# Kernel tuning notes

Measured on AMD Instinct MI355X. Metric: run time of the kernel, lower is better.

The kernel has to match this reference:

```python
import jax, jax.numpy as jnp
import numpy as np

WS = 12      # window_size
OV = 6       # overlap
STEP = WS - OV
EPS = 1e-5   # LayerNorm eps (torch default)


def setup_inputs() -> dict:
    key = jax.random.key(0)
    ks = jax.random.split(key, 6)
    B, L, H, Dh = 4, 4092, 8, 64
    d_model = H * Dh
    sc = 1.0 / np.sqrt(Dh)
    return {
        "queries": jax.random.normal(ks[0], (B, L, H, Dh), dtype=jnp.float32),
        "keys": jax.random.normal(ks[1], (B, L, H, Dh), dtype=jnp.float32),
        "values": jax.random.normal(ks[2], (B, L, H, Dh), dtype=jnp.float32),
        "Wq": jax.random.normal(ks[3], (Dh, Dh), dtype=jnp.float32) * sc,
        "Wk": jax.random.normal(ks[4], (Dh, Dh), dtype=jnp.float32) * sc,
        "Wv": jax.random.normal(ks[5], (Dh, Dh), dtype=jnp.float32) * sc,
        "gamma": jnp.ones((d_model,), dtype=jnp.float32),
        "beta": jnp.zeros((d_model,), dtype=jnp.float32),
    }


def reference(queries, keys, values, Wq, Wk, Wv, gamma, beta):
    # input layout: [B, L, H, Dh]
    B, L, H, Dh = queries.shape
    nw = (L - OV) // STEP                       # number of windows
    Lc = WS + STEP * (nw - 1)                   # reconstructed length (== L)
    idx = jnp.arange(nw)[:, None] * STEP + jnp.arange(WS)[None, :]  # [nw, WS]

    def windows(x):
        # [B,L,H,Dh] -> [B,H,nw,WS,Dh]
        return jnp.transpose(x, (0, 2, 1, 3))[:, :, idx, :]

    qw, kw, vw = windows(queries), windows(keys), windows(values)
    # per-head-dim linear projections (nn.Linear: x @ W.T)
    Q = jnp.einsum('bhnwd,ed->bhnwe', qw, Wq)
    K = jnp.einsum('bhnwd,ed->bhnwe', kw, Wk)
    V = jnp.einsum('bhnwd,ed->bhnwe', vw, Wv)

    scores = jnp.einsum('bhnqd,bhnkd->bhnqk', Q, K) / jnp.sqrt(jnp.asarray(Dh, Q.dtype))
    attn = jax.nn.softmax(scores, axis=-1)      # [B,H,nw,WS,WS]
    ow = jnp.einsum('bhnqk,bhnkd->bhnqd', attn, V)

    # [B,H,nw,WS,Dh] -> [B,nw,WS,H*Dh]
    attn_out = jnp.transpose(ow, (0, 2, 3, 1, 4)).reshape(B, nw, WS, H * Dh)

    # overlap-add + averaging
    flat_idx = idx.reshape(-1)                  # [nw*WS]
    acc = jnp.zeros((B, Lc, H * Dh), dtype=attn_out.dtype)
    acc = acc.at[:, flat_idx, :].add(attn_out.reshape(B, nw * WS, H * Dh))
    cnt = jnp.zeros((Lc,), dtype=attn_out.dtype).at[flat_idx].add(1.0)
    out = acc / cnt[None, :, None]

    # residual + LayerNorm
    resid = queries.reshape(B, L, H * Dh)
    x = out + resid
    mu = jnp.mean(x, axis=-1, keepdims=True)
    var = jnp.mean((x - mu) ** 2, axis=-1, keepdims=True)
    z = (x - mu) / jnp.sqrt(var + EPS) * gamma + beta
    return z, attn
```

## Files before the change

kernel.cpp:

```cpp
#include <hip/hip_runtime.h>
#include <math.h>

#define B_    4
#define L_    4092
#define H_    8
#define DM    512
#define WS_   12
#define NW    681
#define NC    682
#define EPS_  1e-5f
#define Z_ELEMS (B_*L_*DM)
#define NQUAD 32736

typedef unsigned short u16;

__device__ __forceinline__ u16 f2bf(float f) {
    union { float f; unsigned u; } x; x.f = f;
    unsigned u = x.u;
    return (u16)((u + 0x7FFFu + ((u >> 16) & 1u)) >> 16);
}
__device__ __forceinline__ float bf2f(u16 h) {
    union { unsigned u; float f; } x; x.u = ((unsigned)h) << 16; return x.f;
}

__global__ __launch_bounds__(256) void proj_kernel(
    const float* __restrict__ q, const float* __restrict__ k, const float* __restrict__ v,
    const float* __restrict__ Wq, const float* __restrict__ Wk, const float* __restrict__ Wv,
    float* __restrict__ Qf, float* __restrict__ Kf, u16* __restrict__ Vh)
{
    const int tensor = blockIdx.y;
    const float* __restrict__ X = (tensor == 0) ? q  : (tensor == 1) ? k  : v;
    const float* __restrict__ W = (tensor == 0) ? Wq : (tensor == 1) ? Wk : Wv;
    float* __restrict__ Yf      = (tensor == 0) ? Qf : Kf;
    const bool isV = (tensor == 2);

    const int t = threadIdx.x, lane = t & 63, wv = t >> 6;

    float4 wr[16];
    #pragma unroll
    for (int j = 0; j < 16; ++j)
        wr[j] = *(const float4*)(W + lane * 64 + j * 4);

    __shared__ alignas(16) float Xw[4][4][64];

    const int li = lane >> 4;
    const int lc = (lane & 15) * 4;

    const int waveId = blockIdx.x * 4 + wv;
    for (int qd = waveId; qd < NQUAD; qd += 2048) {
        const int rbase = qd * 4;
        const int r = rbase + li;
        const int bh = r / L_;
        const int l = r - bh * L_;
        const int b = bh >> 3, h = bh & 7;
        const float4 xf = *(const float4*)(X + (((size_t)b * L_ + l) * H_ + h) * 64 + lc);
        *(float4*)&Xw[wv][li][lc] = xf;

        float acc0 = 0.f, acc1 = 0.f, acc2 = 0.f, acc3 = 0.f;
        #pragma unroll
        for (int d4 = 0; d4 < 16; ++d4) {
            const float4 w4 = wr[d4];
            const float4 x0 = *(const float4*)&Xw[wv][0][d4 * 4];
            const float4 x1 = *(const float4*)&Xw[wv][1][d4 * 4];
            const float4 x2 = *(const float4*)&Xw[wv][2][d4 * 4];
            const float4 x3 = *(const float4*)&Xw[wv][3][d4 * 4];
            acc0 += x0.x*w4.x + x0.y*w4.y + x0.z*w4.z + x0.w*w4.w;
            acc1 += x1.x*w4.x + x1.y*w4.y + x1.z*w4.z + x1.w*w4.w;
            acc2 += x2.x*w4.x + x2.y*w4.y + x2.z*w4.z + x2.w*w4.w;
            acc3 += x3.x*w4.x + x3.y*w4.y + x3.z*w4.z + x3.w*w4.w;
        }

        const size_t orow = (size_t)rbase * 64 + lane;
        if (!isV) {
            Yf[orow]       = acc0;
            Yf[orow + 64]  = acc1;
            Yf[orow + 128] = acc2;
            Yf[orow + 192] = acc3;
        } else {
            Vh[orow]       = f2bf(acc0);
            Vh[orow + 64]  = f2bf(acc1);
            Vh[orow + 128] = f2bf(acc2);
            Vh[orow + 192] = f2bf(acc3);
        }
    }
}

__global__ __launch_bounds__(512, 4) void attn_ln_kernel(
    const float* __restrict__ Qf, const float* __restrict__ Kf, const u16* __restrict__ Vh,
    const float* __restrict__ qres, const float* __restrict__ gamma,
    const float* __restrict__ beta, float* __restrict__ attn, float* __restrict__ z)
{
    __shared__ alignas(16) float Ks[8][18][64];
    __shared__ alignas(16) float Vsf[8][18][64];

    const int c = blockIdx.x, b = blockIdx.y;
    const int t = threadIdx.x, lane = t & 63, h = t >> 6;
    const int qq = lane >> 2, ks = lane & 3;
    const int bh = b * 8 + h;
    const int lbase = c * 6 - 6;

    for (int i = t; i < 2304; i += 512) {
        const int hh  = i / 288;
        const int rem = i - hh * 288;
        const int rr  = rem >> 4;
        const int cc  = (rem & 15) * 4;
        const int l = lbase + rr;
        float4 kf4 = make_float4(0.f, 0.f, 0.f, 0.f);
        float4 vf4 = make_float4(0.f, 0.f, 0.f, 0.f);
        if (l >= 0 && l < L_) {
            const size_t base = ((size_t)(b * 8 + hh) * L_ + l) * 64 + cc;
            kf4 = *(const float4*)(Kf + base);
            const ushort4 u4 = *(const ushort4*)(Vh + base);
            vf4.x = bf2f(u4.x); vf4.y = bf2f(u4.y); vf4.z = bf2f(u4.z); vf4.w = bf2f(u4.w);
        }
        *(float4*)&Ks[hh][rr][cc]  = kf4;
        *(float4*)&Vsf[hh][rr][cc] = vf4;
    }
    __syncthreads();

    const bool hasA = (c < NW), hasB = (c > 0);
    const float scale = (hasA && hasB) ? 0.5f : 1.0f;

    float4 qs0, qs1, qs2, qs3;
    const int qmax = hasA ? 12 : 6;
    if (qq < qmax) {
        const float* qp = Qf + ((size_t)bh * L_ + (c * 6 + qq)) * 64 + ks * 16;
        qs0 = *(const float4*)(qp);     qs1 = *(const float4*)(qp + 4);
        qs2 = *(const float4*)(qp + 8); qs3 = *(const float4*)(qp + 12);
    } else {
        qs0 = qs1 = qs2 = qs3 = make_float4(0.f, 0.f, 0.f, 0.f);
    }

    float s[18];
    #pragma unroll
    for (int kt = 0; kt < 18; ++kt) {
        const float* kp = &Ks[h][kt][ks * 16];
        const float4 k0 = *(const float4*)(kp);
        const float4 k1 = *(const float4*)(kp + 4);
        const float4 k2 = *(const float4*)(kp + 8);
        const float4 k3 = *(const float4*)(kp + 12);
        s[kt] = qs0.x*k0.x + qs0.y*k0.y + qs0.z*k0.z + qs0.w*k0.w
              + qs1.x*k1.x + qs1.y*k1.y + qs1.z*k1.z + qs1.w*k1.w
              + qs2.x*k2.x + qs2.y*k2.y + qs2.z*k2.z + qs2.w*k2.w
              + qs3.x*k3.x + qs3.y*k3.y + qs3.z*k3.z + qs3.w*k3.w;
    }
    #pragma unroll
    for (int kt = 0; kt < 18; ++kt) {
        s[kt] += __shfl_xor(s[kt], 1);
        s[kt] += __shfl_xor(s[kt], 2);
    }

    float eA[12], invA = 0.f;
    if (hasA) {
        float mxA = s[6];
        #pragma unroll
        for (int j = 1; j < 12; ++j) mxA = fmaxf(mxA, s[6 + j]);
        float sumA = 0.f;
        #pragma unroll
        for (int j = 0; j < 12; ++j) { eA[j] = __expf((s[6 + j] - mxA) * 0.125f); sumA += eA[j]; }
        invA = 1.0f / sumA;
        if (ks == 0 && qq < 12) {
            float* ao = attn + ((size_t)bh * NW + c) * 144 + qq * 12;
            float4 a0, a1, a2;
            a0.x = eA[0]*invA; a0.y = eA[1]*invA;  a0.z = eA[2]*invA;  a0.w = eA[3]*invA;
            a1.x = eA[4]*invA; a1.y = eA[5]*invA;  a1.z = eA[6]*invA;  a1.w = eA[7]*invA;
            a2.x = eA[8]*invA; a2.y = eA[9]*invA;  a2.z = eA[10]*invA; a2.w = eA[11]*invA;
            *(float4*)(ao)     = a0;
            *(float4*)(ao + 4) = a1;
            *(float4*)(ao + 8) = a2;
        }
    } else {
        #pragma unroll
        for (int j = 0; j < 12; ++j) eA[j] = 0.f;
    }

    float eB[12], invB = 0.f;
    if (hasB) {
        float mxB = s[0];
        #pragma unroll
        for (int j = 1; j < 12; ++j) mxB = fmaxf(mxB, s[j]);
        float sumB = 0.f;
        #pragma unroll
        for (int j = 0; j < 12; ++j) { eB[j] = __expf((s[j] - mxB) * 0.125f); sumB += eB[j]; }
        invB = 1.0f / sumB;
    } else {
        #pragma unroll
        for (int j = 0; j < 12; ++j) eB[j] = 0.f;
    }

    float4 xo0 = make_float4(0.f,0.f,0.f,0.f), xo1 = xo0, xo2 = xo0, xo3 = xo0;
    if (qq < 6) {
        #pragma unroll
        for (int kt = 0; kt < 18; ++kt) {
            const float wa = (kt >= 6) ? eA[kt - 6] * invA : 0.f;
            const float wb = (kt < 12) ? eB[kt] * invB : 0.f;
            const float wk = scale * (wa + wb);
            const float* vp = &Vsf[h][kt][ks * 16];
            const float4 v0 = *(const float4*)(vp);
            const float4 v1 = *(const float4*)(vp + 4);
            const float4 v2 = *(const float4*)(vp + 8);
            const float4 v3 = *(const float4*)(vp + 12);
            xo0.x += wk*v0.x; xo0.y += wk*v0.y; xo0.z += wk*v0.z; xo0.w += wk*v0.w;
            xo1.x += wk*v1.x; xo1.y += wk*v1.y; xo1.z += wk*v1.z; xo1.w += wk*v1.w;
            xo2.x += wk*v2.x; xo2.y += wk*v2.y; xo2.z += wk*v2.z; xo2.w += wk*v2.w;
            xo3.x += wk*v3.x; xo3.y += wk*v3.y; xo3.z += wk*v3.z; xo3.w += wk*v3.w;
        }
    }
    __syncthreads();

    float* Xs = &Ks[0][0][0];
    if (qq < 6) {
        float* xp = Xs + qq * 516 + h * 64 + ks * 16;
        *(float4*)(xp)      = xo0;
        *(float4*)(xp + 4)  = xo1;
        *(float4*)(xp + 8)  = xo2;
        *(float4*)(xp + 12) = xo3;
    }
    __syncthreads();

    if (h < 6) {
        const int l = c * 6 + h;
        const int cc = lane * 8;
        float4 xa = *(const float4*)(Xs + h * 516 + cc);
        float4 xb = *(const float4*)(Xs + h * 516 + cc + 4);
        const float* qr = qres + ((size_t)b * L_ + l) * DM + cc;
        const float4 ra  = *(const float4*)qr;
        const float4 rb2 = *(const float4*)(qr + 4);
        xa.x += ra.x;  xa.y += ra.y;  xa.z += ra.z;  xa.w += ra.w;
        xb.x += rb2.x; xb.y += rb2.y; xb.z += rb2.z; xb.w += rb2.w;

        float s1 = xa.x + xa.y + xa.z + xa.w + xb.x + xb.y + xb.z + xb.w;
        float s2 = xa.x*xa.x + xa.y*xa.y + xa.z*xa.z + xa.w*xa.w
                 + xb.x*xb.x + xb.y*xb.y + xb.z*xb.z + xb.w*xb.w;
        #pragma unroll
        for (int off = 1; off < 64; off <<= 1) {
            s1 += __shfl_xor(s1, off, 64);
            s2 += __shfl_xor(s2, off, 64);
        }
        const float mu  = s1 * (1.0f / 512.0f);
        const float var = s2 * (1.0f / 512.0f) - mu * mu;
        const float inv = 1.0f / sqrtf(var + EPS_);

        const float4 ga = *(const float4*)(gamma + cc);
        const float4 gb = *(const float4*)(gamma + cc + 4);
        const float4 ba = *(const float4*)(beta + cc);
        const float4 bb = *(const float4*)(beta + cc + 4);
        float4 oa, ob;
        oa.x = (xa.x - mu) * inv * ga.x + ba.x;
        oa.y = (xa.y - mu) * inv * ga.y + ba.y;
        oa.z = (xa.z - mu) * inv * ga.z + ba.z;
        oa.w = (xa.w - mu) * inv * ga.w + ba.w;
        ob.x = (xb.x - mu) * inv * gb.x + bb.x;
        ob.y = (xb.y - mu) * inv * gb.y + bb.y;
        ob.z = (xb.z - mu) * inv * gb.z + bb.z;
        ob.w = (xb.w - mu) * inv * gb.w + bb.w;
        float* zp = z + ((size_t)b * L_ + l) * DM + cc;
        *(float4*)zp = oa;
        *(float4*)(zp + 4) = ob;
    }
}

extern "C" void kernel_launch(void* const* d_in, const int* in_sizes, int n_in,
                              void* d_out, int out_size, void* d_ws, size_t ws_size,
                              hipStream_t stream) {
    const float* q     = (const float*)d_in[0];
    const float* k     = (const float*)d_in[1];
    const float* v     = (const float*)d_in[2];
    const float* Wq    = (const float*)d_in[3];
    const float* Wk    = (const float*)d_in[4];
    const float* Wv    = (const float*)d_in[5];
    const float* gamma = (const float*)d_in[6];
    const float* beta  = (const float*)d_in[7];

    float* z    = (float*)d_out;
    float* attn = (float*)d_out + Z_ELEMS;

    const size_t plane = (size_t)B_ * H_ * L_ * 64;
    float* Qf = (float*)d_ws;
    float* Kf = Qf + plane;
    u16*  Vh  = (u16*)(Kf + plane);

    proj_kernel<<<dim3(512, 3, 1), 256, 0, stream>>>(q, k, v, Wq, Wk, Wv, Qf, Kf, Vh);
    attn_ln_kernel<<<dim3(NC, B_), 512, 0, stream>>>(Qf, Kf, Vh, q, gamma, beta, attn, z);
}
```

Measured before the change: 247.5 us.

## Split attention and LayerNorm kernels, double-buffer projection loads

The fused attention+LayerNorm kernel is split in two. An attention kernel handles four heads per block over a 3D grid and writes the pre-norm output into z. A separate LayerNorm kernel then reads it back with the residual and normalises it in place. The projection kernel now stages W transposed through shared memory and double-buffers the next input quad to overlap global loads with compute. The split adds a full extra round-trip of z through global memory in exchange for smaller blocks and more parallelism. Holding 64 weight scalars per thread may raise register pressure.

Result: slower. 254.2 us (+2.7%).

```diff
diff --git a/kernel.cpp b/kernel.cpp
--- a/kernel.cpp
+++ b/kernel.cpp
@@ -23,11 +23,23 @@
     union { unsigned u; float f; } x; x.u = ((unsigned)h) << 16; return x.f;
 }
 
+__device__ __forceinline__ float4 load_x4(const float* __restrict__ X,
+                                          int qd, int li, int lc) {
+    const int rbase = qd * 4;
+    const int bh = rbase / L_;
+    const int l0 = rbase - bh * L_;
+    const int b = bh >> 3, h = bh & 7;
+    return *(const float4*)(X + (((size_t)b * L_ + (l0 + li)) * H_ + h) * 64 + lc);
+}
+
 __global__ __launch_bounds__(256) void proj_kernel(
     const float* __restrict__ q, const float* __restrict__ k, const float* __restrict__ v,
     const float* __restrict__ Wq, const float* __restrict__ Wk, const float* __restrict__ Wv,
     float* __restrict__ Qf, float* __restrict__ Kf, u16* __restrict__ Vh)
 {
+    __shared__ float Wt[64][65];
+    __shared__ float Xw[4][2][4][64];
+
     const int tensor = blockIdx.y;
     const float* __restrict__ X = (tensor == 0) ? q  : (tensor == 1) ? k  : v;
     const float* __restrict__ W = (tensor == 0) ? Wq : (tensor == 1) ? Wk : Wv;
@@ -36,41 +48,45 @@
 
     const int t = threadIdx.x, lane = t & 63, wv = t >> 6;
 
-    float4 wr[16];
+    for (int i = t; i < 4096; i += 256)
+        Wt[i & 63][i >> 6] = W[i];
+    __syncthreads();
+
+    float wr[64];
     #pragma unroll
-    for (int j = 0; j < 16; ++j)
-        wr[j] = *(const float4*)(W + lane * 64 + j * 4);
-
-    __shared__ alignas(16) float Xw[4][4][64];
+    for (int d = 0; d < 64; ++d) wr[d] = Wt[d][lane];
 
     const int li = lane >> 4;
     const int lc = (lane & 15) * 4;
 
     const int waveId = blockIdx.x * 4 + wv;
+    int cur = 0;
+    if (waveId < NQUAD) {
+        const float4 x0 = load_x4(X, waveId, li, lc);
+        *(float4*)&Xw[wv][0][li][lc] = x0;
+    }
     for (int qd = waveId; qd < NQUAD; qd += 2048) {
-        const int rbase = qd * 4;
-        const int r = rbase + li;
-        const int bh = r / L_;
-        const int l = r - bh * L_;
-        const int b = bh >> 3, h = bh & 7;
-        const float4 xf = *(const float4*)(X + (((size_t)b * L_ + l) * H_ + h) * 64 + lc);
-        *(float4*)&Xw[wv][li][lc] = xf;
+        const int qn = qd + 2048;
+        const bool pf = (qn < NQUAD);
+        float4 xn = make_float4(0.f, 0.f, 0.f, 0.f);
+        if (pf) xn = load_x4(X, qn, li, lc);
 
         float acc0 = 0.f, acc1 = 0.f, acc2 = 0.f, acc3 = 0.f;
         #pragma unroll
         for (int d4 = 0; d4 < 16; ++d4) {
-            const float4 w4 = wr[d4];
-            const float4 x0 = *(const float4*)&Xw[wv][0][d4 * 4];
-            const float4 x1 = *(const float4*)&Xw[wv][1][d4 * 4];
-            const float4 x2 = *(const float4*)&Xw[wv][2][d4 * 4];
-            const float4 x3 = *(const float4*)&Xw[wv][3][d4 * 4];
-            acc0 += x0.x*w4.x + x0.y*w4.y + x0.z*w4.z + x0.w*w4.w;
-            acc1 += x1.x*w4.x + x1.y*w4.y + x1.z*w4.z + x1.w*w4.w;
-            acc2 += x2.x*w4.x + x2.y*w4.y + x2.z*w4.z + x2.w*w4.w;
-            acc3 += x3.x*w4.x + x3.y*w4.y + x3.z*w4.z + x3.w*w4.w;
-        }
-
-        const size_t orow = (size_t)rbase * 64 + lane;
+            const float4 x0 = *(const float4*)&Xw[wv][cur][0][d4 * 4];
+            const float4 x1 = *(const float4*)&Xw[wv][cur][1][d4 * 4];
+            const float4 x2 = *(const float4*)&Xw[wv][cur][2][d4 * 4];
+            const float4 x3 = *(const float4*)&Xw[wv][cur][3][d4 * 4];
+            const float w0 = wr[4 * d4 + 0], w1 = wr[4 * d4 + 1];
+            const float w2 = wr[4 * d4 + 2], w3 = wr[4 * d4 + 3];
+            acc0 += x0.x*w0 + x0.y*w1 + x0.z*w2 + x0.w*w3;
+            acc1 += x1.x*w0 + x1.y*w1 + x1.z*w2 + x1.w*w3;
+            acc2 += x2.x*w0 + x2.y*w1 + x2.z*w2 + x2.w*w3;
+            acc3 += x3.x*w0 + x3.y*w1 + x3.z*w2 + x3.w*w3;
+        }
+
+        const size_t orow = (size_t)(qd * 4) * 64 + lane;
         if (!isV) {
             Yf[orow]       = acc0;
             Yf[orow + 64]  = acc1;
@@ -82,24 +98,29 @@
             Vh[orow + 128] = f2bf(acc2);
             Vh[orow + 192] = f2bf(acc3);
         }
-    }
-}
-
-__global__ __launch_bounds__(512, 4) void attn_ln_kernel(
+
+        if (pf) {
+            *(float4*)&Xw[wv][cur ^ 1][li][lc] = xn;
+            cur ^= 1;
+        }
+    }
+}
+
+__global__ __launch_bounds__(256, 4) void attn_kernel(
     const float* __restrict__ Qf, const float* __restrict__ Kf, const u16* __restrict__ Vh,
-    const float* __restrict__ qres, const float* __restrict__ gamma,
-    const float* __restrict__ beta, float* __restrict__ attn, float* __restrict__ z)
+    float* __restrict__ attn, float* __restrict__ xout)
 {
-    __shared__ alignas(16) float Ks[8][18][64];
-    __shared__ alignas(16) float Vsf[8][18][64];
-
-    const int c = blockIdx.x, b = blockIdx.y;
-    const int t = threadIdx.x, lane = t & 63, h = t >> 6;
+    __shared__ alignas(16) float Ks[4][18][64];
+    __shared__ alignas(16) float Vs[4][18][64];
+
+    const int c = blockIdx.x, b = blockIdx.y, hg = blockIdx.z;
+    const int t = threadIdx.x, lane = t & 63, w = t >> 6;
+    const int h = hg * 4 + w;
     const int qq = lane >> 2, ks = lane & 3;
     const int bh = b * 8 + h;
     const int lbase = c * 6 - 6;
 
-    for (int i = t; i < 2304; i += 512) {
+    for (int i = t; i < 1152; i += 256) {
         const int hh  = i / 288;
         const int rem = i - hh * 288;
         const int rr  = rem >> 4;
@@ -108,13 +129,13 @@
         float4 kf4 = make_float4(0.f, 0.f, 0.f, 0.f);
         float4 vf4 = make_float4(0.f, 0.f, 0.f, 0.f);
         if (l >= 0 && l < L_) {
-            const size_t base = ((size_t)(b * 8 + hh) * L_ + l) * 64 + cc;
+            const size_t base = ((size_t)(b * 8 + hg * 4 + hh) * L_ + l) * 64 + cc;
             kf4 = *(const float4*)(Kf + base);
             const ushort4 u4 = *(const ushort4*)(Vh + base);
             vf4.x = bf2f(u4.x); vf4.y = bf2f(u4.y); vf4.z = bf2f(u4.z); vf4.w = bf2f(u4.w);
         }
-        *(float4*)&Ks[hh][rr][cc]  = kf4;
-        *(float4*)&Vsf[hh][rr][cc] = vf4;
+        *(float4*)&Ks[hh][rr][cc] = kf4;
+        *(float4*)&Vs[hh][rr][cc] = vf4;
     }
     __syncthreads();
 
@@ -134,7 +155,7 @@
     float s[18];
     #pragma unroll
     for (int kt = 0; kt < 18; ++kt) {
-        const float* kp = &Ks[h][kt][ks * 16];
+        const float* kp = &Ks[w][kt][ks * 16];
         const float4 k0 = *(const float4*)(kp);
         const float4 k1 = *(const float4*)(kp + 4);
         const float4 k2 = *(const float4*)(kp + 8);
@@ -188,14 +209,14 @@
         for (int j = 0; j < 12; ++j) eB[j] = 0.f;
     }
 
-    float4 xo0 = make_float4(0.f,0.f,0.f,0.f), xo1 = xo0, xo2 = xo0, xo3 = xo0;
     if (qq < 6) {
+        float4 xo0 = make_float4(0.f,0.f,0.f,0.f), xo1 = xo0, xo2 = xo0, xo3 = xo0;
         #pragma unroll
         for (int kt = 0; kt < 18; ++kt) {
             const float wa = (kt >= 6) ? eA[kt - 6] * invA : 0.f;
             const float wb = (kt < 12) ? eB[kt] * invB : 0.f;
             const float wk = scale * (wa + wb);
-            const float* vp = &Vsf[h][kt][ks * 16];
+            const float* vp = &Vs[w][kt][ks * 16];
             const float4 v0 = *(const float4*)(vp);
             const float4 v1 = *(const float4*)(vp + 4);
             const float4 v2 = *(const float4*)(vp + 8);
@@ -205,59 +226,58 @@
             xo2.x += wk*v2.x; xo2.y += wk*v2.y; xo2.z += wk*v2.z; xo2.w += wk*v2.w;
             xo3.x += wk*v3.x; xo3.y += wk*v3.y; xo3.z += wk*v3.z; xo3.w += wk*v3.w;
         }
-    }
-    __syncthreads();
-
-    float* Xs = &Ks[0][0][0];
-    if (qq < 6) {
-        float* xp = Xs + qq * 516 + h * 64 + ks * 16;
+        float* xp = xout + ((size_t)b * L_ + (c * 6 + qq)) * DM + h * 64 + ks * 16;
         *(float4*)(xp)      = xo0;
         *(float4*)(xp + 4)  = xo1;
         *(float4*)(xp + 8)  = xo2;
         *(float4*)(xp + 12) = xo3;
     }
-    __syncthreads();
-
-    if (h < 6) {
-        const int l = c * 6 + h;
-        const int cc = lane * 8;
-        float4 xa = *(const float4*)(Xs + h * 516 + cc);
-        float4 xb = *(const float4*)(Xs + h * 516 + cc + 4);
-        const float* qr = qres + ((size_t)b * L_ + l) * DM + cc;
-        const float4 ra  = *(const float4*)qr;
-        const float4 rb2 = *(const float4*)(qr + 4);
-        xa.x += ra.x;  xa.y += ra.y;  xa.z += ra.z;  xa.w += ra.w;
-        xb.x += rb2.x; xb.y += rb2.y; xb.z += rb2.z; xb.w += rb2.w;
-
-        float s1 = xa.x + xa.y + xa.z + xa.w + xb.x + xb.y + xb.z + xb.w;
-        float s2 = xa.x*xa.x + xa.y*xa.y + xa.z*xa.z + xa.w*xa.w
-                 + xb.x*xb.x + xb.y*xb.y + xb.z*xb.z + xb.w*xb.w;
-        #pragma unroll
-        for (int off = 1; off < 64; off <<= 1) {
-            s1 += __shfl_xor(s1, off, 64);
-            s2 += __shfl_xor(s2, off, 64);
-        }
-        const float mu  = s1 * (1.0f / 512.0f);
-        const float var = s2 * (1.0f / 512.0f) - mu * mu;
-        const float inv = 1.0f / sqrtf(var + EPS_);
-
-        const float4 ga = *(const float4*)(gamma + cc);
-        const float4 gb = *(const float4*)(gamma + cc + 4);
-        const float4 ba = *(const float4*)(beta + cc);
-        const float4 bb = *(const float4*)(beta + cc + 4);
-        float4 oa, ob;
-        oa.x = (xa.x - mu) * inv * ga.x + ba.x;
-        oa.y = (xa.y - mu) * inv * ga.y + ba.y;
-        oa.z = (xa.z - mu) * inv * ga.z + ba.z;
-        oa.w = (xa.w - mu) * inv * ga.w + ba.w;
-        ob.x = (xb.x - mu) * inv * gb.x + bb.x;
-        ob.y = (xb.y - mu) * inv * gb.y + bb.y;
-        ob.z = (xb.z - mu) * inv * gb.z + bb.z;
-        ob.w = (xb.w - mu) * inv * gb.w + bb.w;
-        float* zp = z + ((size_t)b * L_ + l) * DM + cc;
-        *(float4*)zp = oa;
-        *(float4*)(zp + 4) = ob;
-    }
+}
+
+__global__ __launch_bounds__(512) void ln_kernel(
+    const float* __restrict__ qres, const float* __restrict__ gamma,
+    const float* __restrict__ beta, float* __restrict__ z)
+{
+    const int row = blockIdx.x * 8 + (threadIdx.x >> 6);
+    const int lane = threadIdx.x & 63;
+    const int cc = lane * 8;
+
+    float* xp = z + (size_t)row * DM + cc;
+    float4 xa = *(const float4*)(xp);
+    float4 xb = *(const float4*)(xp + 4);
+    const float* qr = qres + (size_t)row * DM + cc;
+    const float4 ra  = *(const float4*)qr;
+    const float4 rb2 = *(const float4*)(qr + 4);
+    xa.x += ra.x;  xa.y += ra.y;  xa.z += ra.z;  xa.w += ra.w;
+    xb.x += rb2.x; xb.y += rb2.y; xb.z += rb2.z; xb.w += rb2.w;
+
+    float s1 = xa.x + xa.y + xa.z + xa.w + xb.x + xb.y + xb.z + xb.w;
+    float s2 = xa.x*xa.x + xa.y*xa.y + xa.z*xa.z + xa.w*xa.w
+             + xb.x*xb.x + xb.y*xb.y + xb.z*xb.z + xb.w*xb.w;
+    #pragma unroll
+    for (int off = 1; off < 64; off <<= 1) {
+        s1 += __shfl_xor(s1, off, 64);
+        s2 += __shfl_xor(s2, off, 64);
+    }
+    const float mu  = s1 * (1.0f / 512.0f);
+    const float var = s2 * (1.0f / 512.0f) - mu * mu;
+    const float inv = 1.0f / sqrtf(var + EPS_);
+
+    const float4 ga = *(const float4*)(gamma + cc);
+    const float4 gb = *(const float4*)(gamma + cc + 4);
+    const float4 ba = *(const float4*)(beta + cc);
+    const float4 bb = *(const float4*)(beta + cc + 4);
+    float4 oa, ob;
+    oa.x = (xa.x - mu) * inv * ga.x + ba.x;
+    oa.y = (xa.y - mu) * inv * ga.y + ba.y;
+    oa.z = (xa.z - mu) * inv * ga.z + ba.z;
+    oa.w = (xa.w - mu) * inv * ga.w + ba.w;
+    ob.x = (xb.x - mu) * inv * gb.x + bb.x;
+    ob.y = (xb.y - mu) * inv * gb.y + bb.y;
+    ob.z = (xb.z - mu) * inv * gb.z + bb.z;
+    ob.w = (xb.w - mu) * inv * gb.w + bb.w;
+    *(float4*)(xp)     = oa;
+    *(float4*)(xp + 4) = ob;
 }
 
 extern "C" void kernel_launch(void* const* d_in, const int* in_sizes, int n_in,
@@ -281,5 +301,6 @@
     u16*  Vh  = (u16*)(Kf + plane);
 
     proj_kernel<<<dim3(512, 3, 1), 256, 0, stream>>>(q, k, v, Wq, Wk, Wv, Qf, Kf, Vh);
-    attn_ln_kernel<<<dim3(NC, B_), 512, 0, stream>>>(Qf, Kf, Vh, q, gamma, beta, attn, z);
-}
+    attn_kernel<<<dim3(NC, B_, 2), 256, 0, stream>>>(Qf, Kf, Vh, attn, z);
+    ln_kernel<<<dim3(2046, 1, 1), 512, 0, stream>>>(q, gamma, beta, z);
+}
```
